# Performance work log

Measured on AMD Instinct MI355X. Metric: run time of the kernel, lower is better.

Reference implementation:

```python
import jax, jax.numpy as jnp
import numpy as np

B, N, D = 4, 4096, 1024
STD = 1.0 / D

def setup_inputs() -> dict:
    key = jax.random.key(0)
    ks = jax.random.split(key, 6)
    return {
        "x_real": jax.random.normal(ks[0], (B, N, D), dtype=jnp.float32),
        "x_imag": jax.random.normal(ks[1], (B, N, D), dtype=jnp.float32),
        "w_query_real": jax.random.normal(ks[2], (D, D), dtype=jnp.float32) * STD,
        "w_query_imag": jax.random.normal(ks[3], (D, D), dtype=jnp.float32) * STD,
        "w_key": jax.random.normal(ks[4], (D, D), dtype=jnp.float32) * STD,
        "w_value": jax.random.normal(ks[5], (D, D), dtype=jnp.float32) * STD,
    }

def reference(x_real, x_imag, w_query_real, w_query_imag, w_key, w_value):
    # query gate: (x.real @ Wqr) * (x.imag @ Wqi)  -> [b, n, e]
    query = jnp.einsum('bnd,de->bne', x_real, w_query_real) * \
            jnp.einsum('bnd,de->bne', x_imag, w_query_imag)
    key = jnp.einsum('bnd,de->bne', x_real, w_key)      # [b, n, d]
    value = jnp.einsum('bnd,de->bne', x_imag, w_value)  # [b, n, e]
    # linear-attention style reduction over sequence dim n
    kv_attn = jnp.einsum('bnd,bne->bde', key, value)    # [b, d, e]
    # dropout with p=0.0 (eval / identity)
    bffn = jnp.einsum('bnd,bde->bne', query, kv_attn)   # [b, n, e]
    return bffn
```

## Files before the change

### kernel.cpp

```cpp
#include <hip/hip_runtime.h>
#include <stdint.h>

typedef unsigned short ushort_t;
typedef __attribute__((ext_vector_type(8))) short bf16x8;
typedef __attribute__((ext_vector_type(4))) float f32x4;

__device__ __forceinline__ ushort_t f2bf(float f) {
  union { float f; uint32_t u; } v; v.f = f;
  uint32_t u = v.u;
  u += 0x7FFFu + ((u >> 16) & 1u);
  return (ushort_t)(u >> 16);
}
__device__ __forceinline__ float bf2f(ushort_t h) {
  union { uint32_t u; float f; } v; v.u = ((uint32_t)h) << 16;
  return v.f;
}
__device__ __forceinline__ void gl2lds16(const void* g, void* l) {
  __builtin_amdgcn_global_load_lds(
      (__attribute__((address_space(1))) void*)(uintptr_t)g,
      (__attribute__((address_space(3))) void*)(uint32_t)(uintptr_t)l,
      16, 0, 0);
}


__device__ __forceinline__ void gemm256x128(
    const ushort_t* __restrict__ A, int lda,
    const ushort_t* __restrict__ Bt, int ldb,
    int m0, int n0, int K, char* __restrict__ smem,
    f32x4 (&acc)[4][4]) {
  const int t = threadIdx.x;
  const int nt = K >> 5;
  const int rowS = t >> 2;
  const int kgS = (t & 3) ^ ((t >> 3) & 3);
  const ushort_t* a0 = A + (size_t)(m0 + rowS) * lda + kgS * 8;
  const ushort_t* a1 = a0 + (size_t)128 * lda;
  const ushort_t* b0 = Bt + (size_t)(n0 + rowS) * ldb + kgS * 8;
  const int d0 = t * 16;
  const int lane = t & 63, wid = t >> 6;
  const int wm = wid >> 1, wn = wid & 1;
  const int lr = lane & 15, lq = lane >> 4;
  const int o = lr * 64 + ((lq ^ ((lr >> 1) & 3)) << 4);
  const int aW = wm * 4096;
  const int bW = 16384 + wn * 4096;

#define STAGE(tt, buf) do { \
    char* s = smem + (buf); \
    gl2lds16(a0 + (tt) * 32, s + d0); \
    gl2lds16(a1 + (tt) * 32, s + 8192 + d0); \
    gl2lds16(b0 + (tt) * 32, s + 16384 + d0); \
  } while (0)

  bf16x8 aF[4], bF[4];
  STAGE(0, 0);
  for (int tt = 0; tt < nt; ++tt) {
    asm volatile("s_waitcnt vmcnt(0) lgkmcnt(0)\n\ts_barrier" ::: "memory");
    const int cb = (tt & 1) ? 24576 : 0;
    if (tt + 1 < nt) STAGE(tt + 1, (tt & 1) ? 0 : 24576);
    const char* base = smem + cb;
    #pragma unroll
    for (int mi = 0; mi < 4; ++mi)
      aF[mi] = *(const bf16x8*)(base + aW + mi * 1024 + o);
    #pragma unroll
    for (int ni = 0; ni < 4; ++ni)
      bF[ni] = *(const bf16x8*)(base + bW + ni * 1024 + o);
    __builtin_amdgcn_s_setprio(1);
    #pragma unroll
    for (int mi = 0; mi < 4; ++mi)
      #pragma unroll
      for (int ni = 0; ni < 4; ++ni)
        acc[mi][ni] = __builtin_amdgcn_mfma_f32_16x16x32_bf16(aF[mi], bF[ni], acc[mi][ni], 0, 0, 0);
    __builtin_amdgcn_s_setprio(0);
  }
#undef STAGE
}

__global__ __launch_bounds__(512, 2) void gq(
    const ushort_t* __restrict__ Xr, const ushort_t* __restrict__ Xi,
    const ushort_t* __restrict__ Wr, const ushort_t* __restrict__ Wi,
    ushort_t* __restrict__ Q) {
  extern __shared__ char smem[];
  const int bid = blockIdx.x;
  const int xcd = bid & 7, i = bid >> 3;
  const int m0 = (xcd * 8 + (i >> 3)) * 256;
  const int n0 = (i & 7) * 128;
  const int t = threadIdx.x;
  const int lane = t & 63, wid = t >> 6;
  const int wm = wid >> 1, wn = wid & 1;
  const int lr = lane & 15, lq = lane >> 4;

  const int rowS = t >> 2;
  const int kgS = (t & 3) ^ ((t >> 3) & 3);
  const ushort_t* ar0 = Xr + (size_t)(m0 + rowS) * 1024 + kgS * 8;
  const ushort_t* ar1 = ar0 + (size_t)128 * 1024;
  const ushort_t* ai0 = Xi + (size_t)(m0 + rowS) * 1024 + kgS * 8;
  const ushort_t* ai1 = ai0 + (size_t)128 * 1024;
  const ushort_t* br0 = Wr + (size_t)(n0 + rowS) * 1024 + kgS * 8;
  const ushort_t* bi0 = Wi + (size_t)(n0 + rowS) * 1024 + kgS * 8;
  const int d0 = t * 16;
  const int o = lr * 64 + ((lq ^ ((lr >> 1) & 3)) << 4);
  const int aW = wm * 4096;
  const int bW = 16384 + wn * 4096;

#define STG3(p0, p1, pb, ks, buf) do { \
    char* s = smem + (buf); \
    gl2lds16(p0 + (ks) * 32, s + d0); \
    gl2lds16(p1 + (ks) * 32, s + 8192 + d0); \
    gl2lds16(pb + (ks) * 32, s + 16384 + d0); \
  } while (0)
#define RDFRAG(buf) do { \
    const char* base = smem + (buf); \
    _Pragma("unroll") \
    for (int mi = 0; mi < 4; ++mi) aF[mi] = *(const bf16x8*)(base + aW + mi * 1024 + o); \
    _Pragma("unroll") \
    for (int ni = 0; ni < 4; ++ni) bF[ni] = *(const bf16x8*)(base + bW + ni * 1024 + o); \
  } while (0)
#define MM(ACC) \
    __builtin_amdgcn_s_setprio(1); \
    _Pragma("unroll") \
    for (int mi = 0; mi < 4; ++mi) \
      _Pragma("unroll") \
      for (int ni = 0; ni < 4; ++ni) \
        ACC[mi][ni] = __builtin_amdgcn_mfma_f32_16x16x32_bf16(aF[mi], bF[ni], ACC[mi][ni], 0, 0, 0); \
    __builtin_amdgcn_s_setprio(0);
#define BND() asm volatile("s_waitcnt vmcnt(0) lgkmcnt(0)\n\ts_barrier" ::: "memory")

  f32x4 accR[4][4] = {}, accI[4][4] = {};
  bf16x8 aF[4], bF[4];

  STG3(ar0, ar1, br0, 0, 0);
  for (int ks = 0; ks < 32; ++ks) {
    BND();
    STG3(ai0, ai1, bi0, ks, 24576);
    RDFRAG(0);
    MM(accR)
    BND();
    if (ks + 1 < 32) STG3(ar0, ar1, br0, ks + 1, 0);
    RDFRAG(24576);
    MM(accI)
  }
#undef STG3
#undef RDFRAG
#undef MM
#undef BND

  #pragma unroll
  for (int mi = 0; mi < 4; ++mi) {
    int rbase = m0 + wm * 64 + mi * 16 + lq * 4;
    #pragma unroll
    for (int ni = 0; ni < 4; ++ni) {
      int c = n0 + wn * 64 + ni * 16 + lr;
      #pragma unroll
      for (int r = 0; r < 4; ++r)
        Q[(size_t)(rbase + r) * 1024 + c] = f2bf(accR[mi][ni][r] * accI[mi][ni][r]);
    }
  }
}

__global__ __launch_bounds__(512, 4) void gpart(
    const ushort_t* __restrict__ XrT, const ushort_t* __restrict__ XiT,
    ushort_t* __restrict__ P) {
  extern __shared__ char smem[];
  const int bid = blockIdx.x;
  const int xcd = bid & 7, i = bid >> 3;
  const int z = xcd * 2 + (i >> 5);
  const int mn = i & 31;
  const int m0 = (mn >> 3) * 256, n0 = (mn & 7) * 128;
  const int b = z & 3, s = z >> 2;
  const ushort_t* A = XrT + ((size_t)b << 22) + s * 1024;
  const ushort_t* Bt = XiT + ((size_t)b << 22) + s * 1024;
  f32x4 acc[4][4] = {};
  gemm256x128(A, 4096, Bt, 4096, m0, n0, 1024, smem, acc);

  const int t = threadIdx.x, lane = t & 63, wid = t >> 6;
  const int wm = wid >> 1, wn = wid & 1;
  const int lr = lane & 15, lq = lane >> 4;
  ushort_t* C = P + ((size_t)z << 20);
  #pragma unroll
  for (int mi = 0; mi < 4; ++mi) {
    int rbase = m0 + wm * 64 + mi * 16 + lq * 4;
    #pragma unroll
    for (int ni = 0; ni < 4; ++ni) {
      int c = n0 + wn * 64 + ni * 16 + lr;
      #pragma unroll
      for (int r = 0; r < 4; ++r)
        C[(size_t)(rbase + r) * 1024 + c] = f2bf(acc[mi][ni][r]);
    }
  }
}

__global__ __launch_bounds__(256) void g_reduce(const ushort_t* __restrict__ P,
                                                ushort_t* __restrict__ G) {
  size_t e4 = ((size_t)blockIdx.x * 256 + threadIdx.x) * 4;
  int b = (int)(e4 >> 20);
  size_t j = e4 & ((1u << 20) - 1);
  float s0 = 0.f, s1 = 0.f, s2 = 0.f, s3 = 0.f;
  #pragma unroll
  for (int sp = 0; sp < 4; ++sp) {
    ushort4 v = *(const ushort4*)(P + ((size_t)(sp * 4 + b) << 20) + j);
    s0 += bf2f(v.x); s1 += bf2f(v.y); s2 += bf2f(v.z); s3 += bf2f(v.w);
  }
  *(ushort4*)&G[e4] = make_ushort4(f2bf(s0), f2bf(s1), f2bf(s2), f2bf(s3));
}

__global__ __launch_bounds__(128, 4) void gemm1k(
    const ushort_t* __restrict__ Abase, int aStride,
    const ushort_t* __restrict__ Btbase, int btStride,
    ushort_t* __restrict__ Cbase) {
  extern __shared__ char smem[];
  const int bid = blockIdx.x;
  const int b = bid >> 7, mn = bid & 127;
  const int m0 = (mn >> 4) * 128, n0 = (mn & 15) * 64;
  const ushort_t* A = Abase + (size_t)b * (size_t)aStride;
  const ushort_t* Bt = Btbase + (size_t)b * (size_t)btStride;

  const int t = threadIdx.x;
  const int lane = t & 63, wid = t >> 6;
  const int lr = lane & 15, lq = lane >> 4;

  const ushort_t* pa[4];
  const ushort_t* pb[2];
  int dA[4], dB[2];
  #pragma unroll
  for (int p = 0; p < 4; ++p) {
    int ch = p * 128 + t;
    int row = ch >> 2;
    int kg = (ch & 3) ^ ((row >> 1) & 3);
    pa[p] = A + (size_t)(m0 + row) * 1024 + kg * 8;
    dA[p] = ch * 16;
  }
  #pragma unroll
  for (int p = 0; p < 2; ++p) {
    int ch = p * 128 + t;
    int row = ch >> 2;
    int kg = (ch & 3) ^ ((row >> 1) & 3);
    pb[p] = Bt + (size_t)(n0 + row) * 1024 + kg * 8;
    dB[p] = 8192 + ch * 16;
  }
  const int o = lr * 64 + ((lq ^ ((lr >> 1) & 3)) << 4);
  const int aW = wid * 4096;

#define STG1(tt, buf) do { \
    char* s = smem + (buf); \
    gl2lds16(pa[0] + (tt) * 32, s + dA[0]); \
    gl2lds16(pa[1] + (tt) * 32, s + dA[1]); \
    gl2lds16(pa[2] + (tt) * 32, s + dA[2]); \
    gl2lds16(pa[3] + (tt) * 32, s + dA[3]); \
    gl2lds16(pb[0] + (tt) * 32, s + dB[0]); \
    gl2lds16(pb[1] + (tt) * 32, s + dB[1]); \
  } while (0)

  f32x4 acc[4][4] = {};
  bf16x8 aF[4], bF[4];
  STG1(0, 0);
  for (int tt = 0; tt < 32; ++tt) {
    asm volatile("s_waitcnt vmcnt(0) lgkmcnt(0)\n\ts_barrier" ::: "memory");
    const int cb = (tt & 1) ? 12288 : 0;
    if (tt + 1 < 32) STG1(tt + 1, (tt & 1) ? 0 : 12288);
    const char* base = smem + cb;
    #pragma unroll
    for (int mi = 0; mi < 4; ++mi)
      aF[mi] = *(const bf16x8*)(base + aW + mi * 1024 + o);
    #pragma unroll
    for (int ni = 0; ni < 4; ++ni)
      bF[ni] = *(const bf16x8*)(base + 8192 + ni * 1024 + o);
    __builtin_amdgcn_s_setprio(1);
    #pragma unroll
    for (int mi = 0; mi < 4; ++mi)
      #pragma unroll
      for (int ni = 0; ni < 4; ++ni)
        acc[mi][ni] = __builtin_amdgcn_mfma_f32_16x16x32_bf16(aF[mi], bF[ni], acc[mi][ni], 0, 0, 0);
    __builtin_amdgcn_s_setprio(0);
  }
#undef STG1

  ushort_t* C = Cbase + ((size_t)b << 20);
  #pragma unroll
  for (int mi = 0; mi < 4; ++mi) {
    int rbase = m0 + wid * 64 + mi * 16 + lq * 4;
    #pragma unroll
    for (int ni = 0; ni < 4; ++ni) {
      int c = n0 + ni * 16 + lr;
      #pragma unroll
      for (int r = 0; r < 4; ++r)
        C[(size_t)(rbase + r) * 1024 + c] = f2bf(acc[mi][ni][r]);
    }
  }
}

__global__ __launch_bounds__(512, 4) void fin8(
    const ushort_t* __restrict__ Q, const ushort_t* __restrict__ KVT,
    float* __restrict__ Out) {
  extern __shared__ char smem[];
  const int bid = blockIdx.x;
  const int xcd = bid & 7, i = bid >> 3;
  const int m0 = (xcd * 8 + (i >> 3)) * 256;
  const int n0 = (i & 7) * 128;
  const int b = m0 >> 12;
  f32x4 acc[4][4] = {};
  gemm256x128(Q, 1024, KVT + ((size_t)b << 20), 1024, m0, n0, 1024, smem, acc);

  const int t = threadIdx.x, lane = t & 63, wid = t >> 6;
  const int wm = wid >> 1, wn = wid & 1;
  const int lr = lane & 15, lq = lane >> 4;
  #pragma unroll
  for (int mi = 0; mi < 4; ++mi) {
    int rbase = m0 + wm * 64 + mi * 16 + lq * 4;
    #pragma unroll
    for (int ni = 0; ni < 4; ++ni) {
      int c = n0 + wn * 64 + ni * 16 + lr;
      #pragma unroll
      for (int r = 0; r < 4; ++r)
        Out[(size_t)(rbase + r) * 1024 + c] = acc[mi][ni][r];
    }
  }
}

__global__ __launch_bounds__(256) void prep2(
    const float* __restrict__ xr, const float* __restrict__ xi,
    const float* w0, const float* w1, const float* w2, const float* w3,
    ushort_t* __restrict__ xrb, ushort_t* __restrict__ xib,
    ushort_t* __restrict__ xrT, ushort_t* __restrict__ xiT,
    ushort_t* o0, ushort_t* o1, ushort_t* o2, ushort_t* o3) {
  const int bid = blockIdx.x;
  const int t = threadIdx.x;
  if (bid < 4096) {
    __shared__ float tile[32][33];
    const int tx = t & 31, ty = t >> 5;
    const float* W; ushort_t* O;
    switch (bid >> 10) {
      case 0: W = w0; O = o0; break;
      case 1: W = w1; O = o1; break;
      case 2: W = w2; O = o2; break;
      default: W = w3; O = o3; break;
    }
    const int within = bid & 1023;
    const int bx = (within & 31) * 32, by = (within >> 5) * 32;
    #pragma unroll
    for (int k = 0; k < 32; k += 8)
      tile[ty + k][tx] = W[(size_t)(by + ty + k) * 1024 + bx + tx];
    __syncthreads();
    #pragma unroll
    for (int k = 0; k < 32; k += 8)
      O[(size_t)(bx + ty + k) * 1024 + by + tx] = f2bf(tile[tx][ty + k]);
  } else {
    __shared__ float tx64[64][65];
    const int xb = bid - 4096;
    const int tensor = xb >> 12;
    const int within = xb & 4095;
    const int n0 = (within >> 4) * 64;
    const int d0g = (within & 15) * 64;
    const float* src = tensor ? xi : xr;
    ushort_t* dstS = tensor ? xib : xrb;
    ushort_t* dstT = tensor ? xiT : xrT;
    const int r = t >> 2;
    const int c4 = (t & 3) * 4;
    #pragma unroll
    for (int p = 0; p < 4; ++p) {
      float4 v = *(const float4*)&src[(size_t)(n0 + r) * 1024 + d0g + c4 + p * 16];
      tx64[r][c4 + p * 16 + 0] = v.x;
      tx64[r][c4 + p * 16 + 1] = v.y;
      tx64[r][c4 + p * 16 + 2] = v.z;
      tx64[r][c4 + p * 16 + 3] = v.w;
    }
    __syncthreads();
    {
      const int c0 = (t & 3) * 16;
      ushort_t tmp[16];
      #pragma unroll
      for (int j = 0; j < 16; ++j) tmp[j] = f2bf(tx64[r][c0 + j]);
      ushort_t* p = &dstS[(size_t)(n0 + r) * 1024 + d0g + c0];
      *(bf16x8*)&p[0] = *(const bf16x8*)&tmp[0];
      *(bf16x8*)&p[8] = *(const bf16x8*)&tmp[8];
    }
    {
      const int nb = (t & 3) * 16;
      ushort_t tmp[16];
      #pragma unroll
      for (int j = 0; j < 16; ++j) tmp[j] = f2bf(tx64[nb + j][r]);
      const int b = n0 >> 12, nn = n0 & 4095;
      ushort_t* p = &dstT[((size_t)b << 22) + (size_t)(d0g + r) * 4096 + nn + nb];
      *(bf16x8*)&p[0] = *(const bf16x8*)&tmp[0];
      *(bf16x8*)&p[8] = *(const bf16x8*)&tmp[8];
    }
  }
}

extern "C" void kernel_launch(void* const* d_in, const int* in_sizes, int n_in,
                              void* d_out, int out_size, void* d_ws, size_t ws_size,
                              hipStream_t stream) {
  const float* xr  = (const float*)d_in[0];
  const float* xi  = (const float*)d_in[1];
  const float* wqr = (const float*)d_in[2];
  const float* wqi = (const float*)d_in[3];
  const float* wk  = (const float*)d_in[4];
  const float* wv  = (const float*)d_in[5];

  char* ws = (char*)d_ws;
  const size_t MB = 1024ull * 1024ull;
  ushort_t* WtQR = (ushort_t*)(ws + 0 * MB);
  ushort_t* WtQI = (ushort_t*)(ws + 2 * MB);
  ushort_t* WtK  = (ushort_t*)(ws + 4 * MB);
  ushort_t* WtV  = (ushort_t*)(ws + 6 * MB);
  ushort_t* XrT  = (ushort_t*)(ws + 8 * MB);
  ushort_t* XiT  = (ushort_t*)(ws + 40 * MB);
  ushort_t* Q    = (ushort_t*)(ws + 72 * MB);
  ushort_t* G    = (ushort_t*)(ws + 104 * MB);
  ushort_t* H    = (ushort_t*)(ws + 8 * MB);
  ushort_t* KVT  = (ushort_t*)(ws + 16 * MB);
  ushort_t* Xrb  = (ushort_t*)d_out;
  ushort_t* Xib  = (ushort_t*)((char*)d_out + 32 * MB);
  ushort_t* Pb   = (ushort_t*)d_out;

  static bool inited = false;
  if (!inited) {
    inited = true;
    hipFuncSetAttribute((const void*)&gq,     hipFuncAttributeMaxDynamicSharedMemorySize, 49152);
    hipFuncSetAttribute((const void*)&gpart,  hipFuncAttributeMaxDynamicSharedMemorySize, 49152);
    hipFuncSetAttribute((const void*)&gemm1k, hipFuncAttributeMaxDynamicSharedMemorySize, 24576);
    hipFuncSetAttribute((const void*)&fin8,   hipFuncAttributeMaxDynamicSharedMemorySize, 49152);
  }

  prep2<<<12288, 256, 0, stream>>>(xr, xi, wqr, wqi, wk, wv,
                                   Xrb, Xib, XrT, XiT, WtQR, WtQI, WtK, WtV);
  gq<<<512, 512, 49152, stream>>>(Xrb, Xib, WtQR, WtQI, Q);
  gpart<<<512, 512, 49152, stream>>>(XrT, XiT, Pb);
  g_reduce<<<4096, 256, 0, stream>>>(Pb, G);
  gemm1k<<<512, 128, 24576, stream>>>(WtV, 0, G, 1 << 20, H);
  gemm1k<<<512, 128, 24576, stream>>>(H, 1 << 20, WtK, 0, KVT);
  fin8<<<512, 512, 49152, stream>>>(Q, KVT, (float*)d_out);
}
```

Baseline: 424.0 us.

## Fuse Gram GEMM into query kernel, drop split-K reduce, retile small GEMMs

The query-gate GEMM and the X_r^T X_i Gram GEMM now run as one launch, with 128 extra blocks computing the full-K Gram product directly. This removes the split-K partial buffer and the separate reduce kernel. The query kernel stages both the real and imaginary tiles in one 96KB double buffer and interleaves their MFMAs, so it needs fewer barriers. The two 1k GEMMs move to the 256x128 tile helper with 128 blocks. The trade-off is lower occupancy and parallelism: the Gram blocks each loop over K=4096, which may leave a long tail, and the small GEMMs now launch only 128 blocks.

```diff
diff --git a/kernel.cpp b/kernel.cpp
--- a/kernel.cpp
+++ b/kernel.cpp
@@ -74,74 +74,95 @@
 #undef STAGE
 }
 
-__global__ __launch_bounds__(512, 2) void gq(
+__global__ __launch_bounds__(512, 1) void gqp(
     const ushort_t* __restrict__ Xr, const ushort_t* __restrict__ Xi,
     const ushort_t* __restrict__ Wr, const ushort_t* __restrict__ Wi,
-    ushort_t* __restrict__ Q) {
+    ushort_t* __restrict__ Q,
+    const ushort_t* __restrict__ XrT, const ushort_t* __restrict__ XiT,
+    ushort_t* __restrict__ G) {
   extern __shared__ char smem[];
   const int bid = blockIdx.x;
-  const int xcd = bid & 7, i = bid >> 3;
-  const int m0 = (xcd * 8 + (i >> 3)) * 256;
-  const int n0 = (i & 7) * 128;
   const int t = threadIdx.x;
   const int lane = t & 63, wid = t >> 6;
   const int wm = wid >> 1, wn = wid & 1;
   const int lr = lane & 15, lq = lane >> 4;
-
   const int rowS = t >> 2;
   const int kgS = (t & 3) ^ ((t >> 3) & 3);
+  const int d0 = t * 16;
+  const int o = lr * 64 + ((lq ^ ((lr >> 1) & 3)) << 4);
+
+  if (bid >= 512) {
+    const int j = bid - 512;
+    const int b = j >> 5, mn = j & 31;
+    const int m0 = (mn >> 3) * 256, n0 = (mn & 7) * 128;
+    const ushort_t* A = XrT + ((size_t)b << 22);
+    const ushort_t* Bt = XiT + ((size_t)b << 22);
+    f32x4 acc[4][4] = {};
+    gemm256x128(A, 4096, Bt, 4096, m0, n0, 4096, smem, acc);
+    ushort_t* C = G + ((size_t)b << 20);
+    #pragma unroll
+    for (int mi = 0; mi < 4; ++mi) {
+      int rbase = m0 + wm * 64 + mi * 16 + lq * 4;
+      #pragma unroll
+      for (int ni = 0; ni < 4; ++ni) {
+        int c = n0 + wn * 64 + ni * 16 + lr;
+        #pragma unroll
+        for (int r = 0; r < 4; ++r)
+          C[(size_t)(rbase + r) * 1024 + c] = f2bf(acc[mi][ni][r]);
+      }
+    }
+    return;
+  }
+
+  const int xcd = bid & 7, i = bid >> 3;
+  const int m0 = (xcd * 8 + (i >> 3)) * 256;
+  const int n0 = (i & 7) * 128;
   const ushort_t* ar0 = Xr + (size_t)(m0 + rowS) * 1024 + kgS * 8;
-  const ushort_t* ar1 = ar0 + (size_t)128 * 1024;
+  const ushort_t* ar1 = ar0 + (size_t)(128 * 1024);
   const ushort_t* ai0 = Xi + (size_t)(m0 + rowS) * 1024 + kgS * 8;
-  const ushort_t* ai1 = ai0 + (size_t)128 * 1024;
+  const ushort_t* ai1 = ai0 + (size_t)(128 * 1024);
   const ushort_t* br0 = Wr + (size_t)(n0 + rowS) * 1024 + kgS * 8;
   const ushort_t* bi0 = Wi + (size_t)(n0 + rowS) * 1024 + kgS * 8;
-  const int d0 = t * 16;
-  const int o = lr * 64 + ((lq ^ ((lr >> 1) & 3)) << 4);
-  const int aW = wm * 4096;
-  const int bW = 16384 + wn * 4096;
-
-#define STG3(p0, p1, pb, ks, buf) do { \
+
+#define STGALL(ks, buf) do { \
     char* s = smem + (buf); \
-    gl2lds16(p0 + (ks) * 32, s + d0); \
-    gl2lds16(p1 + (ks) * 32, s + 8192 + d0); \
-    gl2lds16(pb + (ks) * 32, s + 16384 + d0); \
+    gl2lds16(ar0 + (ks) * 32, s + d0); \
+    gl2lds16(ar1 + (ks) * 32, s + 8192 + d0); \
+    gl2lds16(br0 + (ks) * 32, s + 16384 + d0); \
+    gl2lds16(ai0 + (ks) * 32, s + 24576 + d0); \
+    gl2lds16(ai1 + (ks) * 32, s + 32768 + d0); \
+    gl2lds16(bi0 + (ks) * 32, s + 40960 + d0); \
   } while (0)
-#define RDFRAG(buf) do { \
-    const char* base = smem + (buf); \
-    _Pragma("unroll") \
-    for (int mi = 0; mi < 4; ++mi) aF[mi] = *(const bf16x8*)(base + aW + mi * 1024 + o); \
-    _Pragma("unroll") \
-    for (int ni = 0; ni < 4; ++ni) bF[ni] = *(const bf16x8*)(base + bW + ni * 1024 + o); \
-  } while (0)
-#define MM(ACC) \
-    __builtin_amdgcn_s_setprio(1); \
-    _Pragma("unroll") \
-    for (int mi = 0; mi < 4; ++mi) \
-      _Pragma("unroll") \
-      for (int ni = 0; ni < 4; ++ni) \
-        ACC[mi][ni] = __builtin_amdgcn_mfma_f32_16x16x32_bf16(aF[mi], bF[ni], ACC[mi][ni], 0, 0, 0); \
+
+  f32x4 accR[4][4] = {}, accI[4][4] = {};
+  STGALL(0, 0);
+  for (int ks = 0; ks < 32; ++ks) {
+    asm volatile("s_waitcnt vmcnt(0) lgkmcnt(0)\n\ts_barrier" ::: "memory");
+    const int cb = (ks & 1) ? 49152 : 0;
+    if (ks + 1 < 32) STGALL(ks + 1, (ks & 1) ? 0 : 49152);
+    const char* base = smem + cb;
+    bf16x8 aR[4], bR[4], aI[4], bI[4];
+    #pragma unroll
+    for (int mi = 0; mi < 4; ++mi) {
+      aR[mi] = *(const bf16x8*)(base + wm * 4096 + mi * 1024 + o);
+      aI[mi] = *(const bf16x8*)(base + 24576 + wm * 4096 + mi * 1024 + o);
+    }
+    #pragma unroll
+    for (int ni = 0; ni < 4; ++ni) {
+      bR[ni] = *(const bf16x8*)(base + 16384 + wn * 4096 + ni * 1024 + o);
+      bI[ni] = *(const bf16x8*)(base + 40960 + wn * 4096 + ni * 1024 + o);
+    }
+    __builtin_amdgcn_s_setprio(1);
+    #pragma unroll
+    for (int mi = 0; mi < 4; ++mi)
+      #pragma unroll
+      for (int ni = 0; ni < 4; ++ni) {
+        accR[mi][ni] = __builtin_amdgcn_mfma_f32_16x16x32_bf16(aR[mi], bR[ni], accR[mi][ni], 0, 0, 0);
+        accI[mi][ni] = __builtin_amdgcn_mfma_f32_16x16x32_bf16(aI[mi], bI[ni], accI[mi][ni], 0, 0, 0);
+      }
     __builtin_amdgcn_s_setprio(0);
-#define BND() asm volatile("s_waitcnt vmcnt(0) lgkmcnt(0)\n\ts_barrier" ::: "memory")
-
-  f32x4 accR[4][4] = {}, accI[4][4] = {};
-  bf16x8 aF[4], bF[4];
-
-  STG3(ar0, ar1, br0, 0, 0);
-  for (int ks = 0; ks < 32; ++ks) {
-    BND();
-    STG3(ai0, ai1, bi0, ks, 24576);
-    RDFRAG(0);
-    MM(accR)
-    BND();
-    if (ks + 1 < 32) STG3(ar0, ar1, br0, ks + 1, 0);
-    RDFRAG(24576);
-    MM(accI)
-  }
-#undef STG3
-#undef RDFRAG
-#undef MM
-#undef BND
+  }
+#undef STGALL
 
   #pragma unroll
   for (int mi = 0; mi < 4; ++mi) {
@@ -156,130 +177,29 @@
   }
 }
 
-__global__ __launch_bounds__(512, 4) void gpart(
-    const ushort_t* __restrict__ XrT, const ushort_t* __restrict__ XiT,
-    ushort_t* __restrict__ P) {
-  extern __shared__ char smem[];
-  const int bid = blockIdx.x;
-  const int xcd = bid & 7, i = bid >> 3;
-  const int z = xcd * 2 + (i >> 5);
-  const int mn = i & 31;
-  const int m0 = (mn >> 3) * 256, n0 = (mn & 7) * 128;
-  const int b = z & 3, s = z >> 2;
-  const ushort_t* A = XrT + ((size_t)b << 22) + s * 1024;
-  const ushort_t* Bt = XiT + ((size_t)b << 22) + s * 1024;
-  f32x4 acc[4][4] = {};
-  gemm256x128(A, 4096, Bt, 4096, m0, n0, 1024, smem, acc);
-
-  const int t = threadIdx.x, lane = t & 63, wid = t >> 6;
-  const int wm = wid >> 1, wn = wid & 1;
-  const int lr = lane & 15, lq = lane >> 4;
-  ushort_t* C = P + ((size_t)z << 20);
-  #pragma unroll
-  for (int mi = 0; mi < 4; ++mi) {
-    int rbase = m0 + wm * 64 + mi * 16 + lq * 4;
-    #pragma unroll
-    for (int ni = 0; ni < 4; ++ni) {
-      int c = n0 + wn * 64 + ni * 16 + lr;
-      #pragma unroll
-      for (int r = 0; r < 4; ++r)
-        C[(size_t)(rbase + r) * 1024 + c] = f2bf(acc[mi][ni][r]);
-    }
-  }
-}
-
-__global__ __launch_bounds__(256) void g_reduce(const ushort_t* __restrict__ P,
-                                                ushort_t* __restrict__ G) {
-  size_t e4 = ((size_t)blockIdx.x * 256 + threadIdx.x) * 4;
-  int b = (int)(e4 >> 20);
-  size_t j = e4 & ((1u << 20) - 1);
-  float s0 = 0.f, s1 = 0.f, s2 = 0.f, s3 = 0.f;
-  #pragma unroll
-  for (int sp = 0; sp < 4; ++sp) {
-    ushort4 v = *(const ushort4*)(P + ((size_t)(sp * 4 + b) << 20) + j);
-    s0 += bf2f(v.x); s1 += bf2f(v.y); s2 += bf2f(v.z); s3 += bf2f(v.w);
-  }
-  *(ushort4*)&G[e4] = make_ushort4(f2bf(s0), f2bf(s1), f2bf(s2), f2bf(s3));
-}
-
-__global__ __launch_bounds__(128, 4) void gemm1k(
+__global__ __launch_bounds__(512, 2) void h1k(
     const ushort_t* __restrict__ Abase, int aStride,
     const ushort_t* __restrict__ Btbase, int btStride,
     ushort_t* __restrict__ Cbase) {
   extern __shared__ char smem[];
   const int bid = blockIdx.x;
-  const int b = bid >> 7, mn = bid & 127;
-  const int m0 = (mn >> 4) * 128, n0 = (mn & 15) * 64;
+  const int b = bid >> 5, mn = bid & 31;
+  const int m0 = (mn >> 3) * 256, n0 = (mn & 7) * 128;
   const ushort_t* A = Abase + (size_t)b * (size_t)aStride;
   const ushort_t* Bt = Btbase + (size_t)b * (size_t)btStride;
-
-  const int t = threadIdx.x;
-  const int lane = t & 63, wid = t >> 6;
+  f32x4 acc[4][4] = {};
+  gemm256x128(A, 1024, Bt, 1024, m0, n0, 1024, smem, acc);
+
+  const int t = threadIdx.x, lane = t & 63, wid = t >> 6;
+  const int wm = wid >> 1, wn = wid & 1;
   const int lr = lane & 15, lq = lane >> 4;
-
-  const ushort_t* pa[4];
-  const ushort_t* pb[2];
-  int dA[4], dB[2];
-  #pragma unroll
-  for (int p = 0; p < 4; ++p) {
-    int ch = p * 128 + t;
-    int row = ch >> 2;
-    int kg = (ch & 3) ^ ((row >> 1) & 3);
-    pa[p] = A + (size_t)(m0 + row) * 1024 + kg * 8;
-    dA[p] = ch * 16;
-  }
-  #pragma unroll
-  for (int p = 0; p < 2; ++p) {
-    int ch = p * 128 + t;
-    int row = ch >> 2;
-    int kg = (ch & 3) ^ ((row >> 1) & 3);
-    pb[p] = Bt + (size_t)(n0 + row) * 1024 + kg * 8;
-    dB[p] = 8192 + ch * 16;
-  }
-  const int o = lr * 64 + ((lq ^ ((lr >> 1) & 3)) << 4);
-  const int aW = wid * 4096;
-
-#define STG1(tt, buf) do { \
-    char* s = smem + (buf); \
-    gl2lds16(pa[0] + (tt) * 32, s + dA[0]); \
-    gl2lds16(pa[1] + (tt) * 32, s + dA[1]); \
-    gl2lds16(pa[2] + (tt) * 32, s + dA[2]); \
-    gl2lds16(pa[3] + (tt) * 32, s + dA[3]); \
-    gl2lds16(pb[0] + (tt) * 32, s + dB[0]); \
-    gl2lds16(pb[1] + (tt) * 32, s + dB[1]); \
-  } while (0)
-
-  f32x4 acc[4][4] = {};
-  bf16x8 aF[4], bF[4];
-  STG1(0, 0);
-  for (int tt = 0; tt < 32; ++tt) {
-    asm volatile("s_waitcnt vmcnt(0) lgkmcnt(0)\n\ts_barrier" ::: "memory");
-    const int cb = (tt & 1) ? 12288 : 0;
-    if (tt + 1 < 32) STG1(tt + 1, (tt & 1) ? 0 : 12288);
-    const char* base = smem + cb;
-    #pragma unroll
-    for (int mi = 0; mi < 4; ++mi)
-      aF[mi] = *(const bf16x8*)(base + aW + mi * 1024 + o);
-    #pragma unroll
-    for (int ni = 0; ni < 4; ++ni)
-      bF[ni] = *(const bf16x8*)(base + 8192 + ni * 1024 + o);
-    __builtin_amdgcn_s_setprio(1);
-    #pragma unroll
-    for (int mi = 0; mi < 4; ++mi)
-      #pragma unroll
-      for (int ni = 0; ni < 4; ++ni)
-        acc[mi][ni] = __builtin_amdgcn_mfma_f32_16x16x32_bf16(aF[mi], bF[ni], acc[mi][ni], 0, 0, 0);
-    __builtin_amdgcn_s_setprio(0);
-  }
-#undef STG1
-
   ushort_t* C = Cbase + ((size_t)b << 20);
   #pragma unroll
   for (int mi = 0; mi < 4; ++mi) {
-    int rbase = m0 + wid * 64 + mi * 16 + lq * 4;
+    int rbase = m0 + wm * 64 + mi * 16 + lq * 4;
     #pragma unroll
     for (int ni = 0; ni < 4; ++ni) {
-      int c = n0 + ni * 16 + lr;
+      int c = n0 + wn * 64 + ni * 16 + lr;
       #pragma unroll
       for (int r = 0; r < 4; ++r)
         C[(size_t)(rbase + r) * 1024 + c] = f2bf(acc[mi][ni][r]);
@@ -409,23 +329,19 @@
   ushort_t* KVT  = (ushort_t*)(ws + 16 * MB);
   ushort_t* Xrb  = (ushort_t*)d_out;
   ushort_t* Xib  = (ushort_t*)((char*)d_out + 32 * MB);
-  ushort_t* Pb   = (ushort_t*)d_out;
 
   static bool inited = false;
   if (!inited) {
     inited = true;
-    hipFuncSetAttribute((const void*)&gq,     hipFuncAttributeMaxDynamicSharedMemorySize, 49152);
-    hipFuncSetAttribute((const void*)&gpart,  hipFuncAttributeMaxDynamicSharedMemorySize, 49152);
-    hipFuncSetAttribute((const void*)&gemm1k, hipFuncAttributeMaxDynamicSharedMemorySize, 24576);
-    hipFuncSetAttribute((const void*)&fin8,   hipFuncAttributeMaxDynamicSharedMemorySize, 49152);
+    hipFuncSetAttribute((const void*)&gqp,  hipFuncAttributeMaxDynamicSharedMemorySize, 98304);
+    hipFuncSetAttribute((const void*)&h1k,  hipFuncAttributeMaxDynamicSharedMemorySize, 49152);
+    hipFuncSetAttribute((const void*)&fin8, hipFuncAttributeMaxDynamicSharedMemorySize, 49152);
   }
 
   prep2<<<12288, 256, 0, stream>>>(xr, xi, wqr, wqi, wk, wv,
                                    Xrb, Xib, XrT, XiT, WtQR, WtQI, WtK, WtV);
-  gq<<<512, 512, 49152, stream>>>(Xrb, Xib, WtQR, WtQI, Q);
-  gpart<<<512, 512, 49152, stream>>>(XrT, XiT, Pb);
-  g_reduce<<<4096, 256, 0, stream>>>(Pb, G);
-  gemm1k<<<512, 128, 24576, stream>>>(WtV, 0, G, 1 << 20, H);
-  gemm1k<<<512, 128, 24576, stream>>>(H, 1 << 20, WtK, 0, KVT);
+  gqp<<<640, 512, 98304, stream>>>(Xrb, Xib, WtQR, WtQI, Q, XrT, XiT, G);
+  h1k<<<128, 512, 49152, stream>>>(WtV, 0, G, 1 << 20, H);
+  h1k<<<128, 512, 49152, stream>>>(H, 1 << 20, WtK, 0, KVT);
   fin8<<<512, 512, 49152, stream>>>(Q, KVT, (float*)d_out);
 }
```

After: 467.5 us. 10.3% more time.
